# Optimization experiments

Measured on AMD Instinct MI355X. Metric: run time of the kernel, lower is better.

The kernel has to match this reference:

```python
import jax, jax.numpy as jnp
import numpy as np

B, C_IN, C_OUT, A, H, W = 32, 256, 512, 256, 64, 64


def setup_inputs() -> dict:
    key = jax.random.key(0)
    ks = jax.random.split(key, 8)
    s = 0.02
    return {
        "x": jax.random.normal(ks[0], (B, C_IN, H, W), dtype=jnp.float32),
        "g": jax.random.normal(ks[1], (B, C_OUT), dtype=jnp.float32),
        "Wg": jax.random.normal(ks[2], (A, C_OUT), dtype=jnp.float32) * s,
        "bg": jnp.full((A,), 0.1, dtype=jnp.float32),
        "Wx": jax.random.normal(ks[3], (A, C_IN), dtype=jnp.float32) * s,
        "bx": jnp.full((A,), 0.1, dtype=jnp.float32),
        "Wf": jax.random.normal(ks[4], (1, A), dtype=jnp.float32) * s,
        "bf": jnp.full((1,), 0.1, dtype=jnp.float32),
    }


def reference(x, g, Wg, bg, Wx, bx, Wf, bf):
    b, c, h, w = x.shape
    gg = g @ Wg.T + bg                                  # [B, A]
    xf = x.reshape(b, c, h * w)                          # [B, C, HW]
    # Linear_x applied per spatial position (batched instead of python loop)
    nx = jnp.einsum('bcn,ac->bna', xf, Wx) + bx          # [B, HW, A]
    nx = jax.nn.relu(gg[:, None, :] + nx)                # [B, HW, A]
    att = jnp.einsum('bna,a->bn', nx, Wf[0]) + bf[0]     # [B, HW]
    # min-subtract, sum-divide normalization
    att = att - jnp.min(att, axis=1, keepdims=True)
    att = att / jnp.sum(att, axis=1, keepdims=True)
    out = jnp.einsum('bcn,bn->bc', xf, att)              # weighted pooling [B, C]
    return out, att.reshape(b, h, w)
```

## Files before the change

kernel.cpp:

```cpp
#include <hip/hip_runtime.h>
#include <stdint.h>

#define B_   32
#define CIN  256
#define COUT 512
#define A_   256
#define HW_  4096
#define NT   64

typedef short  short8  __attribute__((ext_vector_type(8)));
typedef float  float4_ __attribute__((ext_vector_type(4)));

__device__ __forceinline__ unsigned f2bf(float f) {
    unsigned u = __float_as_uint(f);
    u += 0x7FFFu + ((u >> 16) & 1u);
    return u >> 16;
}
__device__ __forceinline__ float bf2f(unsigned h) {
    return __uint_as_float(h << 16);
}

__global__ __launch_bounds__(256) void prep_kernel(
    const float* __restrict__ g, const float* __restrict__ Wg,
    const float* __restrict__ bg, const float* __restrict__ Wx,
    const float* __restrict__ bx,
    unsigned short* __restrict__ Wxbf, float* __restrict__ ggbx,
    float* __restrict__ P, float* __restrict__ T)
{
    int b = blockIdx.x, t = threadIdx.x;
    int i = b * 256 + t;
    P[i] = 0.f; T[i] = 0.f;

    const float4* src = (const float4*)(Wx + (size_t)i * 8);
    float4 v0 = src[0], v1 = src[1];
    uint4 pk;
    pk.x = f2bf(v0.x) | (f2bf(v0.y) << 16);
    pk.y = f2bf(v0.z) | (f2bf(v0.w) << 16);
    pk.z = f2bf(v1.x) | (f2bf(v1.y) << 16);
    pk.w = f2bf(v1.z) | (f2bf(v1.w) << 16);
    *(uint4*)(Wxbf + (size_t)i * 8) = pk;

    __shared__ float gl[COUT];
    gl[t]       = g[b * COUT + t];
    gl[t + 256] = g[b * COUT + 256 + t];
    __syncthreads();

    float acc0 = bg[t] + bx[t], acc1 = 0.f;
    const float4* wr = (const float4*)(Wg + (size_t)t * COUT);
    #pragma unroll 8
    for (int co = 0; co < COUT / 4; co += 2) {
        float4 wv0 = wr[co],     gv0 = *(const float4*)&gl[co * 4];
        float4 wv1 = wr[co + 1], gv1 = *(const float4*)&gl[co * 4 + 4];
        acc0 += wv0.x * gv0.x + wv0.y * gv0.y + wv0.z * gv0.z + wv0.w * gv0.w;
        acc1 += wv1.x * gv1.x + wv1.y * gv1.y + wv1.z * gv1.z + wv1.w * gv1.w;
    }
    ggbx[b * 256 + t] = acc0 + acc1;
}

__global__ __launch_bounds__(256, 4) void attn_main(
    const float* __restrict__ x, const unsigned short* __restrict__ Wxbf,
    const float* __restrict__ ggbx, const float* __restrict__ Wf,
    const float* __restrict__ bfs,
    float* __restrict__ P, float* __restrict__ T, float* __restrict__ raw)
{
    __shared__ unsigned int xT[NT * 128];
    __shared__ float att_part[4][NT];
    __shared__ float raw_l[NT];

    int bid = blockIdx.x;
    int b = bid >> 6, nt = bid & 63;
    int t = threadIdx.x, w = t >> 6, lane = t & 63;
    int quad = lane >> 4, l15 = lane & 15;

    const float* xb = x + (size_t)b * CIN * HW_ + nt * NT;

    {
        int sub = lane >> 4;
        int n4  = (lane & 15) * 4;
        int cb0 = w * 64 + sub * 8;
        int cb1 = cb0 + 32;
        float4_ v[16];
        #pragma unroll
        for (int j = 0; j < 8; j++)
            v[j] = *(const float4_*)(xb + (size_t)(cb0 + j) * HW_ + n4);
        #pragma unroll
        for (int j = 0; j < 8; j++)
            v[8 + j] = *(const float4_*)(xb + (size_t)(cb1 + j) * HW_ + n4);

        #pragma unroll
        for (int gq = 0; gq < 2; gq++) {
            int q = (gq ? cb1 : cb0) >> 3;
            const float4_* vg = &v[gq * 8];
            #pragma unroll
            for (int r = 0; r < 4; r++) {
                uint4 pk;
                pk.x = f2bf(vg[0][r]) | (f2bf(vg[1][r]) << 16);
                pk.y = f2bf(vg[2][r]) | (f2bf(vg[3][r]) << 16);
                pk.z = f2bf(vg[4][r]) | (f2bf(vg[5][r]) << 16);
                pk.w = f2bf(vg[6][r]) | (f2bf(vg[7][r]) << 16);
                int n = n4 + r;
                *(uint4*)&xT[n * 128 + ((q ^ (n & 31)) << 2)] = pk;
            }
        }
    }

    float ga[4], wfv[4];
    #pragma unroll
    for (int ai = 0; ai < 4; ai++) {
        int a = w * 64 + ai * 16 + l15;
        ga[ai]  = ggbx[b * 256 + a];
        wfv[ai] = Wf[a];
    }
    __syncthreads();

    float4_ acc[4][4];
    #pragma unroll
    for (int mi = 0; mi < 4; mi++)
        #pragma unroll
        for (int ai = 0; ai < 4; ai++)
            acc[mi][ai] = (float4_){0.f, 0.f, 0.f, 0.f};

    for (int k0 = 0; k0 < CIN; k0 += 32) {
        int qk = (k0 >> 3) + quad;
        short8 af[4];
        #pragma unroll
        for (int mi = 0; mi < 4; mi++) {
            int n = mi * 16 + l15;
            af[mi] = *(const short8*)&xT[n * 128 + ((qk ^ (n & 31)) << 2)];
        }
        short8 bfr[4];
        #pragma unroll
        for (int ai = 0; ai < 4; ai++) {
            int a = w * 64 + ai * 16 + l15;
            bfr[ai] = *(const short8*)(Wxbf + (size_t)a * 256 + k0 + quad * 8);
        }
        #pragma unroll
        for (int mi = 0; mi < 4; mi++)
            #pragma unroll
            for (int ai = 0; ai < 4; ai++)
                acc[mi][ai] = __builtin_amdgcn_mfma_f32_16x16x32_bf16(
                    af[mi], bfr[ai], acc[mi][ai], 0, 0, 0);
    }

    #pragma unroll
    for (int mi = 0; mi < 4; mi++) {
        float p[4] = {0.f, 0.f, 0.f, 0.f};
        #pragma unroll
        for (int ai = 0; ai < 4; ai++) {
            #pragma unroll
            for (int r = 0; r < 4; r++) {
                float vv = acc[mi][ai][r] + ga[ai];
                vv = fmaxf(vv, 0.f);
                p[r] = fmaf(vv, wfv[ai], p[r]);
            }
        }
        #pragma unroll
        for (int r = 0; r < 4; r++) {
            #pragma unroll
            for (int off = 1; off < 16; off <<= 1)
                p[r] += __shfl_xor(p[r], off, 16);
        }
        if (l15 == 0) {
            #pragma unroll
            for (int r = 0; r < 4; r++)
                att_part[w][mi * 16 + quad * 4 + r] = p[r];
        }
    }
    __syncthreads();

    if (t < NT) {
        float rv = att_part[0][t] + att_part[1][t] + att_part[2][t] + att_part[3][t] + bfs[0];
        raw[b * HW_ + nt * NT + t] = rv;
        raw_l[t] = rv;
    }
    __syncthreads();

    float pp[4] = {0.f, 0.f, 0.f, 0.f};
    float tt[4] = {0.f, 0.f, 0.f, 0.f};
    {
        int q    = (t & 63) >> 1;
        int half = (t & 1) * 8;
        int nb   = (t >> 6) * 16;
        #pragma unroll
        for (int i = 0; i < 16; i++) {
            int n = nb + i;
            uint2 u = *(const uint2*)((const char*)xT + n * 512 + ((q ^ (n & 31)) << 4) + half);
            float rv = raw_l[n];
            float x0 = bf2f(u.x & 0xFFFFu), x1 = bf2f(u.x >> 16);
            float x2 = bf2f(u.y & 0xFFFFu), x3 = bf2f(u.y >> 16);
            pp[0] = fmaf(x0, rv, pp[0]); tt[0] += x0;
            pp[1] = fmaf(x1, rv, pp[1]); tt[1] += x1;
            pp[2] = fmaf(x2, rv, pp[2]); tt[2] += x2;
            pp[3] = fmaf(x3, rv, pp[3]); tt[3] += x3;
        }
    }
    __syncthreads();
    {
        float* red = (float*)xT;
        float4_* pr = (float4_*)(red + w * 512);
        float4_* tr = (float4_*)(red + w * 512 + 256);
        pr[t & 63] = (float4_){pp[0], pp[1], pp[2], pp[3]};
        tr[t & 63] = (float4_){tt[0], tt[1], tt[2], tt[3]};
        __syncthreads();
        float Pc = red[t] + red[512 + t] + red[1024 + t] + red[1536 + t];
        float Tc = red[256 + t] + red[768 + t] + red[1280 + t] + red[1792 + t];
        atomicAdd(&P[b * 256 + t], Pc);
        atomicAdd(&T[b * 256 + t], Tc);
    }
}

__global__ __launch_bounds__(256) void finalize_kernel(
    const float* __restrict__ raw, const float* __restrict__ P,
    const float* __restrict__ T, float* __restrict__ out)
{
    int b = blockIdx.x, t = threadIdx.x;
    const float* r = raw + (size_t)b * HW_;
    float v[16];
    float mn = 3.4e38f, sm = 0.f;
    #pragma unroll
    for (int i = 0; i < 16; i++) {
        v[i] = r[t + 256 * i];
        mn = fminf(mn, v[i]);
        sm += v[i];
    }
    #pragma unroll
    for (int off = 1; off < 64; off <<= 1) {
        mn = fminf(mn, __shfl_xor(mn, off, 64));
        sm += __shfl_xor(sm, off, 64);
    }
    __shared__ float smn[4], ssm[4];
    int w = t >> 6;
    if ((t & 63) == 0) { smn[w] = mn; ssm[w] = sm; }
    __syncthreads();
    mn = fminf(fminf(smn[0], smn[1]), fminf(smn[2], smn[3]));
    sm = (ssm[0] + ssm[1]) + (ssm[2] + ssm[3]);
    float S = sm - 4096.f * mn;
    float inv = 1.f / S;

    float* att = out + B_ * CIN + (size_t)b * HW_;
    #pragma unroll
    for (int i = 0; i < 16; i++) att[t + 256 * i] = (v[i] - mn) * inv;

    int ic = b * 256 + t;
    out[ic] = (P[ic] - mn * T[ic]) * inv;
}

extern "C" void kernel_launch(void* const* d_in, const int* in_sizes, int n_in,
                              void* d_out, int out_size, void* d_ws, size_t ws_size,
                              hipStream_t stream)
{
    const float* x   = (const float*)d_in[0];
    const float* g   = (const float*)d_in[1];
    const float* Wg  = (const float*)d_in[2];
    const float* bg  = (const float*)d_in[3];
    const float* Wx  = (const float*)d_in[4];
    const float* bx  = (const float*)d_in[5];
    const float* Wf  = (const float*)d_in[6];
    const float* bf  = (const float*)d_in[7];
    float* out = (float*)d_out;

    char* wsb = (char*)d_ws;
    unsigned short* Wxbf = (unsigned short*)wsb;
    float* ggbx = (float*)(wsb + 131072);
    float* P    = ggbx + 8192;
    float* T    = P + 8192;
    float* raw  = T + 8192;

    prep_kernel<<<32, 256, 0, stream>>>(g, Wg, bg, Wx, bx, Wxbf, ggbx, P, T);
    attn_main<<<2048, 256, 0, stream>>>(x, Wxbf, ggbx, Wf, bf, P, T, raw);
    finalize_kernel<<<32, 256, 0, stream>>>(raw, P, T, out);
}
```

Measured before the change: 251.5 us.

## Pre-swizzle bf16 Wx into MFMA fragment order and double-buffer K-loop loads

The prep kernel now writes the bf16 copy of Wx in per-lane MFMA fragment order, handled by extra blocks, so each lane in the main kernel reads contiguous 16-byte chunks with coalesced loads. The main GEMM K-loop is fully unrolled with two register buffers, so the loads for the next K-step are issued while the current step's MFMAs run, hiding global and LDS latency. The cost is more live registers (two fragment sets), which could hurt occupancy under the launch bounds of 4 blocks per SM.

```diff
diff --git a/kernel.cpp b/kernel.cpp
--- a/kernel.cpp
+++ b/kernel.cpp
@@ -24,21 +24,28 @@
     const float* __restrict__ g, const float* __restrict__ Wg,
     const float* __restrict__ bg, const float* __restrict__ Wx,
     const float* __restrict__ bx,
-    unsigned short* __restrict__ Wxbf, float* __restrict__ ggbx,
+    uint4* __restrict__ WxR, float* __restrict__ ggbx,
     float* __restrict__ P, float* __restrict__ T)
 {
-    int b = blockIdx.x, t = threadIdx.x;
+    int t = threadIdx.x;
+    if (blockIdx.x >= 32) {
+        int e = (blockIdx.x - 32) * 256 + t;
+        int lane = e & 63, ai = (e >> 6) & 3, kk = (e >> 8) & 7, w = e >> 11;
+        int a  = w * 64 + ai * 16 + (lane & 15);
+        int kb = kk * 32 + (lane >> 4) * 8;
+        const float4* s = (const float4*)(Wx + (size_t)a * 256 + kb);
+        float4 u0 = s[0], u1 = s[1];
+        uint4 pk;
+        pk.x = f2bf(u0.x) | (f2bf(u0.y) << 16);
+        pk.y = f2bf(u0.z) | (f2bf(u0.w) << 16);
+        pk.z = f2bf(u1.x) | (f2bf(u1.y) << 16);
+        pk.w = f2bf(u1.z) | (f2bf(u1.w) << 16);
+        WxR[e] = pk;
+        return;
+    }
+    int b = blockIdx.x;
     int i = b * 256 + t;
     P[i] = 0.f; T[i] = 0.f;
-
-    const float4* src = (const float4*)(Wx + (size_t)i * 8);
-    float4 v0 = src[0], v1 = src[1];
-    uint4 pk;
-    pk.x = f2bf(v0.x) | (f2bf(v0.y) << 16);
-    pk.y = f2bf(v0.z) | (f2bf(v0.w) << 16);
-    pk.z = f2bf(v1.x) | (f2bf(v1.y) << 16);
-    pk.w = f2bf(v1.z) | (f2bf(v1.w) << 16);
-    *(uint4*)(Wxbf + (size_t)i * 8) = pk;
 
     __shared__ float gl[COUT];
     gl[t]       = g[b * COUT + t];
@@ -58,7 +65,7 @@
 }
 
 __global__ __launch_bounds__(256, 4) void attn_main(
-    const float* __restrict__ x, const unsigned short* __restrict__ Wxbf,
+    const float* __restrict__ x, const char* __restrict__ WxR,
     const float* __restrict__ ggbx, const float* __restrict__ Wf,
     const float* __restrict__ bfs,
     float* __restrict__ P, float* __restrict__ T, float* __restrict__ raw)
@@ -120,27 +127,39 @@
         for (int ai = 0; ai < 4; ai++)
             acc[mi][ai] = (float4_){0.f, 0.f, 0.f, 0.f};
 
-    for (int k0 = 0; k0 < CIN; k0 += 32) {
+    const char* wsl = WxR + w * 32768 + lane * 16;
+    short8 afA[4], bfA[4], afB[4], bfB[4];
+
+    auto LD = [&](short8* af, short8* bf, int k0) {
         int qk = (k0 >> 3) + quad;
-        short8 af[4];
         #pragma unroll
         for (int mi = 0; mi < 4; mi++) {
             int n = mi * 16 + l15;
             af[mi] = *(const short8*)&xT[n * 128 + ((qk ^ (n & 31)) << 2)];
         }
-        short8 bfr[4];
-        #pragma unroll
-        for (int ai = 0; ai < 4; ai++) {
-            int a = w * 64 + ai * 16 + l15;
-            bfr[ai] = *(const short8*)(Wxbf + (size_t)a * 256 + k0 + quad * 8);
-        }
+        const char* wk = wsl + (k0 >> 5) * 4096;
+        #pragma unroll
+        for (int ai = 0; ai < 4; ai++)
+            bf[ai] = *(const short8*)(wk + ai * 1024);
+    };
+    auto MM = [&](short8* af, short8* bf) {
         #pragma unroll
         for (int mi = 0; mi < 4; mi++)
             #pragma unroll
             for (int ai = 0; ai < 4; ai++)
                 acc[mi][ai] = __builtin_amdgcn_mfma_f32_16x16x32_bf16(
-                    af[mi], bfr[ai], acc[mi][ai], 0, 0, 0);
-    }
+                    af[mi], bf[ai], acc[mi][ai], 0, 0, 0);
+    };
+
+    LD(afA, bfA, 0);   LD(afB, bfB, 32);
+    MM(afA, bfA);      LD(afA, bfA, 64);
+    MM(afB, bfB);      LD(afB, bfB, 96);
+    MM(afA, bfA);      LD(afA, bfA, 128);
+    MM(afB, bfB);      LD(afB, bfB, 160);
+    MM(afA, bfA);      LD(afA, bfA, 192);
+    MM(afB, bfB);      LD(afB, bfB, 224);
+    MM(afA, bfA);
+    MM(afB, bfB);
 
     #pragma unroll
     for (int mi = 0; mi < 4; mi++) {
@@ -260,13 +279,13 @@
     float* out = (float*)d_out;
 
     char* wsb = (char*)d_ws;
-    unsigned short* Wxbf = (unsigned short*)wsb;
+    uint4* WxR  = (uint4*)wsb;
     float* ggbx = (float*)(wsb + 131072);
     float* P    = ggbx + 8192;
     float* T    = P + 8192;
     float* raw  = T + 8192;
 
-    prep_kernel<<<32, 256, 0, stream>>>(g, Wg, bg, Wx, bx, Wxbf, ggbx, P, T);
-    attn_main<<<2048, 256, 0, stream>>>(x, Wxbf, ggbx, Wf, bf, P, T, raw);
+    prep_kernel<<<64, 256, 0, stream>>>(g, Wg, bg, Wx, bx, WxR, ggbx, P, T);
+    attn_main<<<2048, 256, 0, stream>>>(x, (const char*)WxR, ggbx, Wf, bf, P, T, raw);
     finalize_kernel<<<32, 256, 0, stream>>>(raw, P, T, out);
 }
```

Result: faster. 242.8 us (-3.5%).
